# Kernel tuning notes

Hardware: AMD Instinct MI355X
Metric: run time of the kernel (lower is better)

The kernel has to match this reference:

```python
import jax, jax.numpy as jnp
import numpy as np

B, S, L = 2048, 1024, 32
NEG = -10000.0


def setup_inputs() -> dict:
    key = jax.random.key(0)
    k1, k2, k3, k4 = jax.random.split(key, 4)
    lstm_scores = jax.random.normal(k1, (B, S, L), dtype=jnp.float32)
    word_seq_lens = jax.random.randint(k2, (B,), 1, S + 1)  # lengths in [1, S]
    tags = jax.random.randint(k3, (B, S), 0, L - 3)  # real labels only
    mask = (jnp.arange(S)[None, :] < word_seq_lens[:, None])
    start_idx, end_idx, pad_idx = L - 1, L - 2, L - 3
    transition = jax.random.normal(k4, (L, L), dtype=jnp.float32)
    transition = (transition.at[:, start_idx].set(NEG)
                  .at[end_idx, :].set(NEG)
                  .at[:, pad_idx].set(NEG)
                  .at[pad_idx, :].set(NEG))
    return {"lstm_scores": lstm_scores, "transition": transition,
            "word_seq_lens": word_seq_lens, "tags": tags, "mask": mask}


def _crf_scores(lstm_scores, transition, word_seq_lens, tags, mask):
    b, s, l = lstm_scores.shape
    start_idx, end_idx = l - 1, l - 2

    # ---- forward algorithm (log partition) ----
    # all_scores[b,t,i,j] = transition[i,j] + lstm_scores[b,t,j]; fused into the scan step.
    alpha0 = transition[start_idx][None, :] + lstm_scores[:, 0, :]  # (B,L)

    def step(alpha_prev, emit_t):  # emit_t: (B,L)
        a = jax.nn.logsumexp(alpha_prev[:, :, None] + transition[None, :, :]
                             + emit_t[:, None, :], axis=1)  # (B,L)
        return a, a

    emits = jnp.swapaxes(lstm_scores, 0, 1)  # (S,B,L)
    _, alphas_rest = jax.lax.scan(step, alpha0, emits[1:])
    alphas = jnp.concatenate([alpha0[None], alphas_rest], axis=0)  # (S,B,L)

    last_alpha = alphas[word_seq_lens - 1, jnp.arange(b), :]  # (B,L)
    last_alpha = last_alpha + transition[:, end_idx][None, :]
    unlabeled = jnp.sum(jax.nn.logsumexp(last_alpha, axis=1))

    # ---- gold path score ----
    emit_at_tag = jnp.take_along_axis(lstm_scores, tags[:, :, None], axis=2)[..., 0]  # (B,S)
    begin = transition[start_idx, tags[:, 0]] + emit_at_tag[:, 0]  # (B,)
    trans_mid = transition[tags[:, :-1], tags[:, 1:]]  # (B,S-1)
    middle = trans_mid + emit_at_tag[:, 1:]  # (B,S-1)
    middle = jnp.where(mask[:, 1:], middle, 0.0)
    end_tags = tags[jnp.arange(b), word_seq_lens - 1]  # (B,)
    end = transition[end_tags, end_idx]  # (B,)
    labeled = jnp.sum(begin) + jnp.sum(middle) + jnp.sum(end)

    return unlabeled, labeled


def reference(lstm_scores, transition, word_seq_lens, tags, mask):
    return _crf_scores(lstm_scores, transition, word_seq_lens, tags, mask)
```

## Files before the change

### kernel.cpp

```cpp
#include <hip/hip_runtime.h>

#define NB 2048
#define NS 1024
#define NL 32

static __device__ __forceinline__ float fexp2(float x) {
#if __has_builtin(__builtin_amdgcn_exp2f)
  return __builtin_amdgcn_exp2f(x);
#else
  float r; asm("v_exp_f32 %0, %1" : "=v"(r) : "v"(x)); return r;
#endif
}
static __device__ __forceinline__ float flog2(float x) {
#if __has_builtin(__builtin_amdgcn_logf)
  return __builtin_amdgcn_logf(x);
#else
  float r; asm("v_log_f32 %0, %1" : "=v"(r) : "v"(x)); return r;
#endif
}

template<int K>
static __device__ __forceinline__ int roti(int x) {
  if constexpr (K == 0) return x;
  else return __builtin_amdgcn_update_dpp(0, x, 0x120 | K, 0xf, 0xf, true);
}
template<int K>
static __device__ __forceinline__ float rotf(float x) {
  return __int_as_float(roti<K>(__float_as_int(x)));
}

static __device__ __forceinline__ float plswap16_sum(float part) {
  float x, y;
  asm volatile("v_mov_b32 %0, %2\n\t"
               "v_mov_b32 %1, %2\n\t"
               "s_nop 1\n\t"
               "v_permlane16_swap_b32 %0, %1\n\t"
               "s_nop 1"
               : "=&v"(x), "=&v"(y) : "v"(part));
  return x + y;
}
static __device__ __forceinline__ float plswap32_sum(float part) {
  float x, y;
  asm volatile("v_mov_b32 %0, %2\n\t"
               "v_mov_b32 %1, %2\n\t"
               "s_nop 1\n\t"
               "v_permlane32_swap_b32 %0, %1\n\t"
               "s_nop 1"
               : "=&v"(x), "=&v"(y) : "v"(part));
  return x + y;
}
static __device__ __forceinline__ int plswap16_partner(int lane) {
  int x, y;
  asm volatile("v_mov_b32 %0, %2\n\t"
               "v_mov_b32 %1, %2\n\t"
               "s_nop 1\n\t"
               "v_permlane16_swap_b32 %0, %1\n\t"
               "s_nop 1"
               : "=&v"(x), "=&v"(y) : "v"(lane));
  return x + y - lane;
}

static __device__ __forceinline__ float tree16(float p, const float* E) {
  float a0 = p * E[0];
  float a1 = rotf<1>(p) * E[1];
  float a2 = rotf<2>(p) * E[2];
  float a3 = rotf<3>(p) * E[3];
  a0 = fmaf(rotf<4>(p),  E[4],  a0);
  a1 = fmaf(rotf<5>(p),  E[5],  a1);
  a2 = fmaf(rotf<6>(p),  E[6],  a2);
  a3 = fmaf(rotf<7>(p),  E[7],  a3);
  a0 = fmaf(rotf<8>(p),  E[8],  a0);
  a1 = fmaf(rotf<9>(p),  E[9],  a1);
  a2 = fmaf(rotf<10>(p), E[10], a2);
  a3 = fmaf(rotf<11>(p), E[11], a3);
  a0 = fmaf(rotf<12>(p), E[12], a0);
  a1 = fmaf(rotf<13>(p), E[13], a1);
  a2 = fmaf(rotf<14>(p), E[14], a2);
  a3 = fmaf(rotf<15>(p), E[15], a3);
  return (a0 + a1) + (a2 + a3);
}

__global__ void zero_out_k(float* out) {
  if (threadIdx.x < 2) out[threadIdx.x] = 0.0f;
}

__global__ __launch_bounds__(128, 2)
void crf_fwd(const float* __restrict__ scores, const float* __restrict__ trans,
             const int* __restrict__ lens, const int* __restrict__ tags,
             float* __restrict__ out)
{
  constexpr float LOG2E = 1.4426950408889634f;
  constexpr float LN2   = 0.6931471805599453f;
  __shared__ float Tld[NL * NL];
  __shared__ float slotm[64];

  const int b    = blockIdx.x;
  const int tid  = threadIdx.x;
  const int wid  = tid >> 6;
  const int lane = tid & 63;
  const int len  = lens[b];
  const int m    = len >> 1;
  const int nB   = len - 1 - m;
  const int r = lane >> 4, c = lane & 15;
  const int labA = c + ((r & 1) << 4);

  const int p16 = plswap16_partner(lane);
  const bool plOK = ((p16 & 15) == c) && ((((p16 >> 4) ^ r) & 1) == 1);
  const int pmax = (lane > p16) ? lane : p16;
  const int labB = plOK ? (c + ((pmax >= 48) ? 16 : 0))
                        : (c + (((r >> 1) & 1) << 4));

  const float* sbf = scores + (size_t)b * (NS * NL);

  for (int k2 = tid; k2 < NL * NL; k2 += 128) Tld[k2] = trans[k2] * LOG2E;
  __syncthreads();

#define COMB16(S) (plOK ? plswap16_sum(S) : ((S) + __shfl_xor((S), 16)))
#define LDROW(DST, ROW, LAB) do { \
    int r_ = (ROW); r_ = r_ < 0 ? 0 : r_; r_ = r_ > len - 1 ? len - 1 : r_; \
    DST = sbf[(size_t)r_ * NL + (LAB)]; \
  } while (0)

  float u, ls;
  bool endB = false;

  if (wid == 0) {
    float EA[16], EB[16];
#define CFA(K) EA[K] = fexp2(Tld[roti<K>(labA) * NL + labB]);
#define CFB(K) EB[K] = fexp2(Tld[roti<K>(labB) * NL + labA]);
    CFA(0)  CFA(1)  CFA(2)  CFA(3)  CFA(4)  CFA(5)  CFA(6)  CFA(7)
    CFA(8)  CFA(9)  CFA(10) CFA(11) CFA(12) CFA(13) CFA(14) CFA(15)
    CFB(0)  CFB(1)  CFB(2)  CFB(3)  CFB(4)  CFB(5)  CFB(6)  CFB(7)
    CFB(8)  CFB(9)  CFB(10) CFB(11) CFB(12) CFB(13) CFB(14) CFB(15)
#undef CFA
#undef CFB
    float a0 = Tld[31 * NL + labA] + LOG2E * sbf[labA];
    ls = __int_as_float(__builtin_amdgcn_readfirstlane(__float_as_int(a0)));
    u = fexp2(a0 - ls);

#define RENORM do { \
    const int eb_ = __builtin_amdgcn_readfirstlane(__float_as_int(u)); \
    const int ex_ = (eb_ >> 23) - 127; \
    ls += (float)ex_; \
    u *= __int_as_float((127 - ex_) << 23); \
  } while (0)

    float P0, P1, P2, P3, Q0, Q1, Q2, Q3;
    int t = 1;
    LDROW(P0, 1, labB); LDROW(P1, 2, labA); LDROW(P2, 3, labB); LDROW(P3, 4, labA);
    LDROW(Q0, 5, labB); LDROW(Q1, 6, labA); LDROW(Q2, 7, labB); LDROW(Q3, 8, labA);

#define FBODY(B0, B1, B2, B3) do { \
    RENORM; \
    const float w0 = fexp2(B0 * LOG2E); \
    const float w1 = fexp2(B1 * LOG2E); \
    const float w2 = fexp2(B2 * LOG2E); \
    const float w3 = fexp2(B3 * LOG2E); \
    LDROW(B0, t + 8,  labB); LDROW(B1, t + 9,  labA); \
    LDROW(B2, t + 10, labB); LDROW(B3, t + 11, labA); \
    u = COMB16(tree16(u, EA)) * w0; \
    u = plswap32_sum(tree16(u, EB)) * w1; \
    u = COMB16(tree16(u, EA)) * w2; \
    u = plswap32_sum(tree16(u, EB)) * w3; \
  } while (0)

    while (t + 7 <= m) {
      FBODY(P0, P1, P2, P3); t += 4;
      FBODY(Q0, Q1, Q2, Q3); t += 4;
    }
    if (t + 3 <= m) { FBODY(P0, P1, P2, P3); t += 4; }
    while (t <= m) {
      if ((t & 3) == 1) RENORM;
      if (t & 1) {
        float e; LDROW(e, t, labB);
        u = COMB16(tree16(u, EA)) * fexp2(e * LOG2E);
        endB = true;
      } else {
        float e; LDROW(e, t, labA);
        u = plswap32_sum(tree16(u, EB)) * fexp2(e * LOG2E);
        endB = false;
      }
      t++;
    }
#undef FBODY
  } else {
    float EA[16], EB[16];
#define CBA(K) EA[K] = fexp2(Tld[labB * NL + roti<K>(labA)]);
#define CBB(K) EB[K] = fexp2(Tld[labA * NL + roti<K>(labB)]);
    CBA(0)  CBA(1)  CBA(2)  CBA(3)  CBA(4)  CBA(5)  CBA(6)  CBA(7)
    CBA(8)  CBA(9)  CBA(10) CBA(11) CBA(12) CBA(13) CBA(14) CBA(15)
    CBB(0)  CBB(1)  CBB(2)  CBB(3)  CBB(4)  CBB(5)  CBB(6)  CBB(7)
    CBB(8)  CBB(9)  CBB(10) CBB(11) CBB(12) CBB(13) CBB(14) CBB(15)
#undef CBA
#undef CBB
    float a0 = Tld[labA * NL + 30];
    ls = __int_as_float(__builtin_amdgcn_readfirstlane(__float_as_int(a0)));
    u = fexp2(a0 - ls);

#define RENORMB do { \
    const int eb_ = __builtin_amdgcn_readfirstlane(__float_as_int(u)); \
    const int ex_ = (eb_ >> 23) - 127; \
    ls += (float)ex_; \
    u *= __int_as_float((127 - ex_) << 23); \
  } while (0)

    float P0, P1, P2, P3, Q0, Q1, Q2, Q3;
    int k = 0;
    LDROW(P0, len - 1, labA); LDROW(P1, len - 2, labB);
    LDROW(P2, len - 3, labA); LDROW(P3, len - 4, labB);
    LDROW(Q0, len - 5, labA); LDROW(Q1, len - 6, labB);
    LDROW(Q2, len - 7, labA); LDROW(Q3, len - 8, labB);

#define BBODY(B0, B1, B2, B3) do { \
    RENORMB; \
    const float w0 = fexp2(B0 * LOG2E); \
    const float w1 = fexp2(B1 * LOG2E); \
    const float w2 = fexp2(B2 * LOG2E); \
    const float w3 = fexp2(B3 * LOG2E); \
    LDROW(B0, len - 1 - k - 8,  labA); LDROW(B1, len - 2 - k - 8,  labB); \
    LDROW(B2, len - 3 - k - 8,  labA); LDROW(B3, len - 4 - k - 8,  labB); \
    u = COMB16(tree16(u * w0, EA)); \
    u = plswap32_sum(tree16(u * w1, EB)); \
    u = COMB16(tree16(u * w2, EA)); \
    u = plswap32_sum(tree16(u * w3, EB)); \
  } while (0)

    while (k + 7 < nB) {
      BBODY(P0, P1, P2, P3); k += 4;
      BBODY(Q0, Q1, Q2, Q3); k += 4;
    }
    if (k + 3 < nB) { BBODY(P0, P1, P2, P3); k += 4; }
    while (k < nB) {
      if ((k & 3) == 0) RENORMB;
      if (!(k & 1)) {
        float e; LDROW(e, len - 1 - k, labA);
        u = COMB16(tree16(u * fexp2(e * LOG2E), EA));
        endB = true;
      } else {
        float e; LDROW(e, len - 1 - k, labB);
        u = plswap32_sum(tree16(u * fexp2(e * LOG2E), EB));
        endB = false;
      }
      k++;
    }
#undef BBODY
#undef RENORMB
  }

  slotm[wid * 32 + (endB ? labB : labA)] = ls + flog2(u);
  __syncthreads();

  if (wid == 0) {
    float v2 = (lane < 32) ? (slotm[lane] + slotm[32 + lane]) : -3.0e38f;
    float mm = v2;
    #pragma unroll
    for (int w = 32; w; w >>= 1) mm = fmaxf(mm, __shfl_xor(mm, w));
    float ssum = fexp2(v2 - mm);
    #pragma unroll
    for (int w = 32; w; w >>= 1) ssum += __shfl_xor(ssum, w);
    if (lane == 0) atomicAdd(out + 0, LN2 * (mm + flog2(ssum)));

    const int* tb = tags + (size_t)b * NS;
    float lab = 0.0f;
    if (lane == 0) {
      const int tg0 = tb[0];
      lab += Tld[31 * NL + tg0] + LOG2E * sbf[tg0];
      const int tgl = tb[len - 1];
      lab += Tld[tgl * NL + 30];
    }
    for (int t2 = 1 + lane; t2 < len; t2 += 64) {
      const int tp = tb[t2 - 1];
      const int tg = tb[t2];
      lab += Tld[tp * NL + tg] + LOG2E * sbf[(size_t)t2 * NL + tg];
    }
    #pragma unroll
    for (int w = 32; w; w >>= 1) lab += __shfl_xor(lab, w);
    if (lane == 0) atomicAdd(out + 1, LN2 * lab);
  }
#undef COMB16
#undef LDROW
#undef RENORM
}

extern "C" void kernel_launch(void* const* d_in, const int* in_sizes, int n_in,
                              void* d_out, int out_size, void* d_ws, size_t ws_size,
                              hipStream_t stream) {
  const float* scores = (const float*)d_in[0];
  const float* trans  = (const float*)d_in[1];
  const int*   lens   = (const int*)d_in[2];
  const int*   tags   = (const int*)d_in[3];
  float* out = (float*)d_out;

  zero_out_k<<<1, 64, 0, stream>>>(out);
  crf_fwd<<<NB, 128, 0, stream>>>(scores, trans, lens, tags, out);
}
```

Measured before the change: 147.6 us.

## Schedule sequences longest-first via device counting-sort permutation

```diff
diff --git a/kernel.cpp b/kernel.cpp
--- a/kernel.cpp
+++ b/kernel.cpp
@@ -84,17 +84,43 @@
   if (threadIdx.x < 2) out[threadIdx.x] = 0.0f;
 }
 
+__global__ __launch_bounds__(1024)
+void sort_perm_k(const int* __restrict__ lens, int* __restrict__ perm) {
+  __shared__ int h0[1024], h1[1024];
+  const int tid = threadIdx.x;
+  h0[tid] = 0;
+  __syncthreads();
+  for (int i = tid; i < NB; i += 1024) atomicAdd(&h0[1024 - lens[i]], 1);
+  __syncthreads();
+  const int cnt = h0[tid];
+  int* src = h0; int* dst = h1;
+  for (int off = 1; off < 1024; off <<= 1) {
+    dst[tid] = src[tid] + ((tid >= off) ? src[tid - off] : 0);
+    __syncthreads();
+    int* tmp = src; src = dst; dst = tmp;
+  }
+  const int excl = src[tid] - cnt;
+  __syncthreads();
+  dst[tid] = excl;
+  __syncthreads();
+  for (int i = tid; i < NB; i += 1024) {
+    const int key = 1024 - lens[i];
+    const int pos = atomicAdd(&dst[key], 1);
+    perm[pos] = i;
+  }
+}
+
 __global__ __launch_bounds__(128, 2)
 void crf_fwd(const float* __restrict__ scores, const float* __restrict__ trans,
              const int* __restrict__ lens, const int* __restrict__ tags,
-             float* __restrict__ out)
+             const int* __restrict__ perm, float* __restrict__ out)
 {
   constexpr float LOG2E = 1.4426950408889634f;
   constexpr float LN2   = 0.6931471805599453f;
   __shared__ float Tld[NL * NL];
   __shared__ float slotm[64];
 
-  const int b    = blockIdx.x;
+  const int b    = perm ? perm[blockIdx.x] : blockIdx.x;
   const int tid  = threadIdx.x;
   const int wid  = tid >> 6;
   const int lane = tid & 63;
@@ -291,6 +317,9 @@
   const int*   tags   = (const int*)d_in[3];
   float* out = (float*)d_out;
 
+  int* perm = (ws_size >= NB * sizeof(int)) ? (int*)d_ws : nullptr;
+
   zero_out_k<<<1, 64, 0, stream>>>(out);
-  crf_fwd<<<NB, 128, 0, stream>>>(scores, trans, lens, tags, out);
-}
+  if (perm) sort_perm_k<<<1, 1024, 0, stream>>>(lens, perm);
+  crf_fwd<<<NB, 128, 0, stream>>>(scores, trans, lens, tags, perm, out);
+}
```

Result: faster. 129.5 us (-12.2%).
